# Kernel optimization log

Measured on AMD Instinct MI355X. Metric: run time of the kernel, lower is better.

## Reference

```python
import jax, jax.numpy as jnp
import numpy as np

N_NODES = 100000
N_EDGES = 1200000


def setup_inputs() -> dict:
    key = jax.random.key(0)
    k1, k2, k3, k4 = jax.random.split(key, 4)
    x = jax.random.normal(k1, (N_NODES, 64), dtype=jnp.float32)
    edge_index = jax.random.randint(k2, (2, N_EDGES), 0, N_NODES, dtype=jnp.int64)
    W1 = jax.random.normal(k3, (64, 64), dtype=jnp.float32) * (1.0 / np.sqrt(64))
    b1 = jnp.zeros((64,), dtype=jnp.float32)
    W2 = jax.random.normal(k4, (64, 32), dtype=jnp.float32) * (1.0 / np.sqrt(64))
    b2 = jnp.zeros((32,), dtype=jnp.float32)
    return {"x": x, "edge_index": edge_index, "W1": W1, "b1": b1, "W2": W2, "b2": b2}


def _gcn_layer(x, src, dst, norm, W, b, n_nodes):
    # x: [N, Fin]; src/dst: [E'] (with self-loops); norm: [E']
    h = x @ W                      # [N, Fout] -- linear transform first (PyG GCNConv)
    msg = h[src] * norm[:, None]   # gather + edge-wise scale, [E', Fout]
    out = jax.ops.segment_sum(msg, dst, num_segments=n_nodes)  # scatter-add
    return out + b


def _gcn_norm(edge_index, n_nodes):
    # add self-loops, then symmetric normalization D^{-1/2} A_hat D^{-1/2}
    loop = jnp.arange(n_nodes, dtype=edge_index.dtype)
    src = jnp.concatenate([edge_index[0], loop])
    dst = jnp.concatenate([edge_index[1], loop])
    ones = jnp.ones(src.shape[0], dtype=jnp.float32)
    deg = jax.ops.segment_sum(ones, dst, num_segments=n_nodes)  # in-degree incl. self-loop
    dinv = jnp.where(deg > 0, jax.lax.rsqrt(deg), 0.0)
    norm = dinv[src] * dinv[dst]
    return src, dst, norm


def reference(x, edge_index, W1, b1, W2, b2):
    n_nodes = x.shape[0]
    src, dst, norm = _gcn_norm(edge_index, n_nodes)
    h = _gcn_layer(x, src, dst, norm, W1, b1, n_nodes)   # op1: GCNConv(in, hidden)
    out = _gcn_layer(h, src, dst, norm, W2, b2, n_nodes) # op2: GCNConv(hidden, out)
    return out
```

## Files before the change

### kernel.cpp

```cpp
#include <hip/hip_runtime.h>


#define TPB 256
#define NPB 512
#define BCAP 8192
#define TILE_E 4096
#define W_ELL 20
#define EXT_W 24
#define OVCAP 512

typedef __attribute__((ext_vector_type(8))) short bf16x8;
typedef __attribute__((ext_vector_type(4))) float f32x4;

__device__ __forceinline__ float bf2f(unsigned short u) {
    unsigned int v = ((unsigned int)u) << 16;
    return __builtin_bit_cast(float, v);
}
__device__ __forceinline__ unsigned short f2bf(float f) {
    unsigned int u = __builtin_bit_cast(unsigned int, f);
    u += 0x7FFFu + ((u >> 16) & 1u);
    return (unsigned short)(u >> 16);
}
__device__ __forceinline__ int edge_val(const void* ei, int is64, long long idx) {
    if (is64) return (int)((const long long*)ei)[idx];
    return ((const int*)ei)[idx];
}

__global__ void k_detect(const unsigned int* __restrict__ w, int nelems, int* flag,
                         int* __restrict__ bucket_wp, int* __restrict__ ext_cnt,
                         unsigned short* __restrict__ T0b, unsigned short* __restrict__ T1b,
                         float* __restrict__ dinv, int n_nodes,
                         const float* __restrict__ W1, const float* __restrict__ W2,
                         const float* __restrict__ b1,
                         unsigned short* __restrict__ W12Tb, float* __restrict__ c1) {
    int t = threadIdx.x;
    if (blockIdx.x == 1) {
        __shared__ float W1s[64][64];
        __shared__ float W2s[64][32];
        for (int i = t; i < 4096; i += TPB) W1s[i >> 6][i & 63] = W1[i];
        for (int i = t; i < 2048; i += TPB) W2s[i >> 5][i & 31] = W2[i];
        __syncthreads();
        for (int i = t; i < 2048; i += TPB) {
            int f = i >> 6, k = i & 63;
            float acc = 0.f;
#pragma unroll
            for (int j = 0; j < 64; ++j) acc += W1s[k][j] * W2s[j][f];
            W12Tb[i] = f2bf(acc);
        }
        if (t < 32) {
            float acc = 0.f;
#pragma unroll
            for (int j = 0; j < 64; ++j) acc += b1[j] * W2s[j][t];
            c1[t] = acc;
        }
        return;
    }
    __shared__ unsigned int red[TPB];
    bucket_wp[t] = 0;
    if (t == 0) {
        *ext_cnt = 0;
        dinv[n_nodes] = 0.f;
    }
    if (t < 32) {
        T0b[(size_t)n_nodes * 32 + t] = 0;
        T1b[(size_t)n_nodes * 32 + t] = 0;
    }
    unsigned int acc = 0;
    int limit = nelems < 16384 ? nelems : 16384;
    for (int i = 1 + 2 * t; i < limit; i += 2 * TPB) acc |= w[i];
    red[t] = acc;
    __syncthreads();
    for (int s = TPB / 2; s > 0; s >>= 1) {
        if (t < s) red[t] |= red[t + s];
        __syncthreads();
    }
    if (t == 0) *flag = (red[0] == 0u) ? 1 : 0;
}

__launch_bounds__(512)
__global__ void k_binA(const void* __restrict__ ei, const int* __restrict__ flag, int E,
                       int nb, unsigned int* __restrict__ gstage, int* __restrict__ bucket_wp) {
    __shared__ int lcnt[256];
    __shared__ int lboff[256];
    __shared__ int lrank[256];
    __shared__ int gbase[256];
    __shared__ int sh[256];
    __shared__ unsigned int spair[TILE_E];
    __shared__ unsigned char sbuck[TILE_E];
    int is64 = *flag;
    int t = threadIdx.x;
    int base_e = blockIdx.x * TILE_E;
    int ne = E - base_e;
    if (ne > TILE_E) ne = TILE_E;

    if (t < 256) {
        lcnt[t] = 0;
        lrank[t] = 0;
    }
    __syncthreads();

    int myb[8];
    unsigned int mypair[8];
#pragma unroll
    for (int k = 0; k < 8; ++k) {
        int idx = t + k * 512;
        myb[k] = -1;
        if (idx < ne) {
            long long e = base_e + idx;
            int s = edge_val(ei, is64, e);
            int d = edge_val(ei, is64, (long long)E + e);
            int b = d >> 9;
            myb[k] = b;
            mypair[k] = (unsigned int)s | ((unsigned int)(d & (NPB - 1)) << 20);
            atomicAdd(&lcnt[b], 1);
        }
    }
    __syncthreads();

    int v0 = (t < 256) ? lcnt[t] : 0;
    if (t < 256) sh[t] = v0;
    __syncthreads();
    for (int st = 1; st < 256; st <<= 1) {
        int u = (t >= st && t < 256) ? sh[t - st] : 0;
        __syncthreads();
        if (t < 256) sh[t] += u;
        __syncthreads();
    }
    if (t < 256) {
        lboff[t] = sh[t] - v0;
        if (t < nb && v0 > 0) gbase[t] = atomicAdd(&bucket_wp[t], v0);
    }
    __syncthreads();

#pragma unroll
    for (int k = 0; k < 8; ++k) {
        int b = myb[k];
        if (b >= 0) {
            int r = atomicAdd(&lrank[b], 1);
            int slot = lboff[b] + r;
            spair[slot] = mypair[k];
            sbuck[slot] = (unsigned char)b;
        }
    }
    __syncthreads();

    for (int j = t; j < ne; j += 512) {
        int b = sbuck[j];
        int pos = gbase[b] + (j - lboff[b]);
        if (pos < BCAP) gstage[(size_t)b * BCAP + pos] = spair[j];
    }
}

__launch_bounds__(512)
__global__ void k_ellB(const unsigned int* __restrict__ gstage, const int* __restrict__ bucket_wp,
                       const float* __restrict__ x, const unsigned short* __restrict__ W12Tb,
                       int* __restrict__ ell, int* __restrict__ cnt, int* __restrict__ ext,
                       int* __restrict__ ext_cnt, float* __restrict__ dinv,
                       unsigned short* __restrict__ T0b, int n_nodes) {
    __shared__ int lrank[NPB];
    __shared__ int slab[NPB * W_ELL];
    __shared__ int exts[NPB];
    __shared__ float sdinv[NPB];
    __shared__ unsigned int ovfl[OVCAP];
    __shared__ int novf;
    int b = blockIdx.x, t = threadIdx.x;
    int zr = n_nodes;
    lrank[t] = 0;
    if (t == 0) novf = 0;
    int4 z4 = make_int4(zr, zr, zr, zr);
    for (int j = t; j < NPB * W_ELL / 4; j += 512) ((int4*)slab)[j] = z4;
    __syncthreads();
    int cb = bucket_wp[b];
    if (cb > BCAP) cb = BCAP;
    const unsigned int* gp = gstage + (size_t)b * BCAP;
    for (int j = t; j < cb; j += 512) {
        unsigned int w = gp[j];
        int dl = (int)(w >> 20);
        int r = atomicAdd(&lrank[dl], 1);
        if (r < W_ELL) {
            slab[dl * W_ELL + r] = (int)(w & 0xFFFFFu);
        } else {
            int o = atomicAdd(&novf, 1);
            if (o < OVCAP) ovfl[o] = w;
        }
    }
    __syncthreads();
    int node = b * NPB + t;
    int deg = lrank[t];
    int extrow = -1;
    if (node < n_nodes && deg > W_ELL) extrow = atomicAdd(ext_cnt, 1);
    exts[t] = extrow;
    float di = (node < n_nodes) ? rsqrtf((float)(deg + 1)) : 0.f;
    sdinv[t] = di;
    if (node < n_nodes) {
        cnt[node] = deg | ((extrow + 1) << 16);
        dinv[node] = di;
    }
    if (extrow >= 0) {
        int4* xp = (int4*)(ext + (size_t)extrow * EXT_W);
#pragma unroll
        for (int j = 0; j < EXT_W / 4; ++j) xp[j] = z4;
    }
    __syncthreads();
    lrank[t] = 0;
    __syncthreads();
    int nov = novf < OVCAP ? novf : OVCAP;
    for (int j = t; j < nov; j += 512) {
        unsigned int w = ovfl[j];
        int dl = (int)(w >> 20);
        int r2 = atomicAdd(&lrank[dl], 1);
        if (r2 < EXT_W) ext[(size_t)exts[dl] * EXT_W + r2] = (int)(w & 0xFFFFFu);
    }
    {
        int4* dst = (int4*)(ell + (size_t)b * (NPB * W_ELL));
        for (int j = t; j < NPB * W_ELL / 4; j += 512) dst[j] = ((int4*)slab)[j];
    }

    int w = t >> 6, lane = t & 63;
    int r = lane & 15, kb = lane >> 4;
#pragma unroll
    for (int ti = 0; ti < 4; ++ti) {
        int lbase = (w * 4 + ti) * 16;
        int nbase = b * NPB + lbase;
        if (nbase >= n_nodes) break;
        int ar = nbase + r;
        if (ar > n_nodes - 1) ar = n_nodes - 1;
        const float* xp = x + (size_t)ar * 64 + kb * 8;
        float4 v0 = ((const float4*)xp)[0];
        float4 v1 = ((const float4*)xp)[1];
        float4 v2 = ((const float4*)(xp + 32))[0];
        float4 v3 = ((const float4*)(xp + 32))[1];
        union { bf16x8 v; unsigned short e[8]; } a0, a1;
        a0.e[0] = f2bf(v0.x); a0.e[1] = f2bf(v0.y); a0.e[2] = f2bf(v0.z); a0.e[3] = f2bf(v0.w);
        a0.e[4] = f2bf(v1.x); a0.e[5] = f2bf(v1.y); a0.e[6] = f2bf(v1.z); a0.e[7] = f2bf(v1.w);
        a1.e[0] = f2bf(v2.x); a1.e[1] = f2bf(v2.y); a1.e[2] = f2bf(v2.z); a1.e[3] = f2bf(v2.w);
        a1.e[4] = f2bf(v3.x); a1.e[5] = f2bf(v3.y); a1.e[6] = f2bf(v3.z); a1.e[7] = f2bf(v3.w);
        int rl = lbase + 4 * kb;
        float d0 = sdinv[rl], d1 = sdinv[rl + 1], d2 = sdinv[rl + 2], d3 = sdinv[rl + 3];
        int rnode = b * NPB + rl;
#pragma unroll
        for (int ft = 0; ft < 2; ++ft) {
            const unsigned short* bp = W12Tb + (size_t)(ft * 16 + r) * 64 + kb * 8;
            bf16x8 b0 = *(const bf16x8*)bp;
            bf16x8 b1v = *(const bf16x8*)(bp + 32);
            f32x4 acc = {0.f, 0.f, 0.f, 0.f};
            acc = __builtin_amdgcn_mfma_f32_16x16x32_bf16(a0.v, b0, acc, 0, 0, 0);
            acc = __builtin_amdgcn_mfma_f32_16x16x32_bf16(a1.v, b1v, acc, 0, 0, 0);
            if (rnode + 0 < n_nodes) T0b[(size_t)(rnode + 0) * 32 + ft * 16 + r] = f2bf(acc[0] * d0);
            if (rnode + 1 < n_nodes) T0b[(size_t)(rnode + 1) * 32 + ft * 16 + r] = f2bf(acc[1] * d1);
            if (rnode + 2 < n_nodes) T0b[(size_t)(rnode + 2) * 32 + ft * 16 + r] = f2bf(acc[2] * d2);
            if (rnode + 3 < n_nodes) T0b[(size_t)(rnode + 3) * 32 + ft * 16 + r] = f2bf(acc[3] * d3);
        }
    }
}

#define GATH32(TBL, S)                                                         \
    {                                                                          \
        ushort4 u = ((const ushort4*)(TBL + (size_t)(S) * 32))[fl];            \
        a0 += bf2f(u.x); a1 += bf2f(u.y); a2 += bf2f(u.z); a3 += bf2f(u.w);    \
    }

__launch_bounds__(TPB)
__global__ void k_agg1(const int* __restrict__ ell, const int* __restrict__ ext,
                       const unsigned short* __restrict__ T0b, const float* __restrict__ dinv,
                       const int* __restrict__ cnt, unsigned short* __restrict__ T1b,
                       float* __restrict__ sraw, int n_nodes) {
    int t = threadIdx.x;
    int lane = t & 63;
    int g = lane >> 3, fl = lane & 7;
    int node = blockIdx.x * 32 + (t >> 6) * 8 + g;
    if (node >= n_nodes) return;
    int cw = cnt[node];
    int cv = cw & 0xFFFF;
    int er = (cw >> 16) - 1;
    const int* epi = ell + (size_t)node * W_ELL;
    const int4* ep = (const int4*)epi;
    int4 i0 = ep[0], i1 = ep[1], i2 = ep[2], i3 = ep[3];
    float sv = dinv[epi[fl]] + dinv[epi[8 + fl]];
    if (fl < 4) sv += dinv[epi[16 + fl]];
    ushort4 su = ((const ushort4*)(T0b + (size_t)node * 32))[fl];
    float a0 = bf2f(su.x), a1 = bf2f(su.y), a2 = bf2f(su.z), a3 = bf2f(su.w);
    GATH32(T0b, i0.x) GATH32(T0b, i0.y) GATH32(T0b, i0.z) GATH32(T0b, i0.w)
    GATH32(T0b, i1.x) GATH32(T0b, i1.y) GATH32(T0b, i1.z) GATH32(T0b, i1.w)
    GATH32(T0b, i2.x) GATH32(T0b, i2.y) GATH32(T0b, i2.z) GATH32(T0b, i2.w)
    GATH32(T0b, i3.x) GATH32(T0b, i3.y) GATH32(T0b, i3.z) GATH32(T0b, i3.w)
    if (__any(cv > 16)) {
        int4 i4 = ep[4];
        GATH32(T0b, i4.x) GATH32(T0b, i4.y) GATH32(T0b, i4.z) GATH32(T0b, i4.w)
    }
    if (er >= 0) {
        const int* xpi = ext + (size_t)er * EXT_W;
        const int4* xp = (const int4*)xpi;
        sv += dinv[xpi[fl]] + dinv[xpi[8 + fl]] + dinv[xpi[16 + fl]];
        int4 e0 = xp[0], e1 = xp[1], e2 = xp[2];
        int4 e3 = xp[3], e4 = xp[4], e5 = xp[5];
        GATH32(T0b, e0.x) GATH32(T0b, e0.y) GATH32(T0b, e0.z) GATH32(T0b, e0.w)
        GATH32(T0b, e1.x) GATH32(T0b, e1.y) GATH32(T0b, e1.z) GATH32(T0b, e1.w)
        GATH32(T0b, e2.x) GATH32(T0b, e2.y) GATH32(T0b, e2.z) GATH32(T0b, e2.w)
        GATH32(T0b, e3.x) GATH32(T0b, e3.y) GATH32(T0b, e3.z) GATH32(T0b, e3.w)
        GATH32(T0b, e4.x) GATH32(T0b, e4.y) GATH32(T0b, e4.z) GATH32(T0b, e4.w)
        GATH32(T0b, e5.x) GATH32(T0b, e5.y) GATH32(T0b, e5.z) GATH32(T0b, e5.w)
    }
    sv += __shfl_xor(sv, 1);
    sv += __shfl_xor(sv, 2);
    sv += __shfl_xor(sv, 4);
    float di = dinv[node];
    float d2 = di * di;
    ushort4 o;
    o.x = f2bf(d2 * a0);
    o.y = f2bf(d2 * a1);
    o.z = f2bf(d2 * a2);
    o.w = f2bf(d2 * a3);
    ((ushort4*)(T1b + (size_t)node * 32))[fl] = o;
    if (fl == 0) sraw[node] = sv + di;
}

__launch_bounds__(TPB)
__global__ void k_agg2(const int* __restrict__ ell, const int* __restrict__ ext,
                       const unsigned short* __restrict__ T1b, const float* __restrict__ dinv,
                       const int* __restrict__ cnt, const float* __restrict__ sraw,
                       const float* __restrict__ c1, const float* __restrict__ b2,
                       float* __restrict__ out, int n_nodes) {
    int t = threadIdx.x;
    int lane = t & 63;
    int g = lane >> 3, fl = lane & 7;
    int node = blockIdx.x * 32 + (t >> 6) * 8 + g;
    if (node >= n_nodes) return;
    int cw = cnt[node];
    int cv = cw & 0xFFFF;
    int er = (cw >> 16) - 1;
    const int4* ep = (const int4*)(ell + (size_t)node * W_ELL);
    int4 i0 = ep[0], i1 = ep[1], i2 = ep[2], i3 = ep[3];
    ushort4 su = ((const ushort4*)(T1b + (size_t)node * 32))[fl];
    float a0 = bf2f(su.x), a1 = bf2f(su.y), a2 = bf2f(su.z), a3 = bf2f(su.w);
    GATH32(T1b, i0.x) GATH32(T1b, i0.y) GATH32(T1b, i0.z) GATH32(T1b, i0.w)
    GATH32(T1b, i1.x) GATH32(T1b, i1.y) GATH32(T1b, i1.z) GATH32(T1b, i1.w)
    GATH32(T1b, i2.x) GATH32(T1b, i2.y) GATH32(T1b, i2.z) GATH32(T1b, i2.w)
    GATH32(T1b, i3.x) GATH32(T1b, i3.y) GATH32(T1b, i3.z) GATH32(T1b, i3.w)
    if (__any(cv > 16)) {
        int4 i4 = ep[4];
        GATH32(T1b, i4.x) GATH32(T1b, i4.y) GATH32(T1b, i4.z) GATH32(T1b, i4.w)
    }
    if (er >= 0) {
        const int4* xp = (const int4*)(ext + (size_t)er * EXT_W);
        int4 e0 = xp[0], e1 = xp[1], e2 = xp[2];
        int4 e3 = xp[3], e4 = xp[4], e5 = xp[5];
        GATH32(T1b, e0.x) GATH32(T1b, e0.y) GATH32(T1b, e0.z) GATH32(T1b, e0.w)
        GATH32(T1b, e1.x) GATH32(T1b, e1.y) GATH32(T1b, e1.z) GATH32(T1b, e1.w)
        GATH32(T1b, e2.x) GATH32(T1b, e2.y) GATH32(T1b, e2.z) GATH32(T1b, e2.w)
        GATH32(T1b, e3.x) GATH32(T1b, e3.y) GATH32(T1b, e3.z) GATH32(T1b, e3.w)
        GATH32(T1b, e4.x) GATH32(T1b, e4.y) GATH32(T1b, e4.z) GATH32(T1b, e4.w)
        GATH32(T1b, e5.x) GATH32(T1b, e5.y) GATH32(T1b, e5.z) GATH32(T1b, e5.w)
    }
    float di = dinv[node];
    float sv = sraw[node];
    float4 cc = ((const float4*)c1)[fl];
    float4 bb = ((const float4*)b2)[fl];
    float4 o;
    o.x = di * (a0 + sv * cc.x) + bb.x;
    o.y = di * (a1 + sv * cc.y) + bb.y;
    o.z = di * (a2 + sv * cc.z) + bb.z;
    o.w = di * (a3 + sv * cc.w) + bb.w;
    ((float4*)(out + (size_t)node * 32))[fl] = o;
}

extern "C" void kernel_launch(void* const* d_in, const int* in_sizes, int n_in,
                              void* d_out, int out_size, void* d_ws, size_t ws_size,
                              hipStream_t stream) {
    const float* x  = (const float*)d_in[0];
    const void*  ei = d_in[1];
    const float* W1 = (const float*)d_in[2];
    const float* b1 = (const float*)d_in[3];
    const float* W2 = (const float*)d_in[4];
    const float* b2 = (const float*)d_in[5];
    float* out = (float*)d_out;

    const int n_nodes = in_sizes[0] / 64;
    const int E = in_sizes[1] / 2;
    const int nb = (n_nodes + NPB - 1) / NPB;

    char* p = (char*)d_ws;
    auto carve = [&](size_t bytes) {
        char* r = p;
        p += (bytes + 255) / 256 * 256;
        return r;
    };
    int* flag      = (int*)carve(sizeof(int));
    int* bucket_wp = (int*)carve(256 * sizeof(int));
    int* ext_cnt   = (int*)carve(sizeof(int));
    int* cnt       = (int*)carve((size_t)n_nodes * sizeof(int));
    float* dinv    = (float*)carve(((size_t)n_nodes + 1) * sizeof(float));
    float* sraw    = (float*)carve((size_t)n_nodes * sizeof(float));
    unsigned int* gstage = (unsigned int*)carve((size_t)nb * BCAP * sizeof(unsigned int));
    int* ell       = (int*)carve((size_t)nb * NPB * W_ELL * sizeof(int));
    int* ext       = (int*)carve((size_t)16384 * EXT_W * sizeof(int));
    unsigned short* T0b = (unsigned short*)carve(((size_t)n_nodes + 1) * 32 * sizeof(unsigned short));
    unsigned short* T1b = (unsigned short*)carve(((size_t)n_nodes + 1) * 32 * sizeof(unsigned short));
    unsigned short* W12Tb = (unsigned short*)carve(32 * 64 * sizeof(unsigned short));
    float* c1      = (float*)carve(32 * sizeof(float));

    k_detect<<<2, TPB, 0, stream>>>((const unsigned int*)ei, in_sizes[1], flag, bucket_wp,
                                    ext_cnt, T0b, T1b, dinv, n_nodes, W1, W2, b1, W12Tb, c1);
    k_binA<<<(E + TILE_E - 1) / TILE_E, 512, 0, stream>>>(ei, flag, E, nb, gstage, bucket_wp);
    k_ellB<<<nb, 512, 0, stream>>>(gstage, bucket_wp, x, W12Tb, ell, cnt, ext, ext_cnt,
                                   dinv, T0b, n_nodes);
    k_agg1<<<(n_nodes + 31) / 32, TPB, 0, stream>>>(ell, ext, T0b, dinv, cnt, T1b, sraw,
                                                    n_nodes);
    k_agg2<<<(n_nodes + 31) / 32, TPB, 0, stream>>>(ell, ext, T1b, dinv, cnt, sraw, c1,
                                                    b2, out, n_nodes);
}
```

Baseline: 95.53 us.

## Drop detect kernel, fold weight prep into ELL build, widen gather lanes

Removes the separate detect kernel. Index width is now detected per block inside the binning kernel, the counters are zeroed with a memset, and every ELL block recomputes the W1·W2 product into shared memory instead of reading it from a global buffer. The aggregation kernels now have each lane gather 8 bf16 features (16-byte loads) with 4 lanes per node, so each block covers 64 nodes instead of 32. This saves a launch and halves the number of gather instructions per edge, at the cost of redundant small matmuls in every ELL block and more registers per lane.

Result: slower. 110.9 us (+16.0%).

```diff
diff --git a/kernel.cpp b/kernel.cpp
--- a/kernel.cpp
+++ b/kernel.cpp
@@ -10,6 +10,7 @@
 #define OVCAP 512
 
 typedef __attribute__((ext_vector_type(8))) short bf16x8;
+typedef __attribute__((ext_vector_type(8))) unsigned short u16x8;
 typedef __attribute__((ext_vector_type(4))) float f32x4;
 
 __device__ __forceinline__ float bf2f(unsigned short u) {
@@ -26,60 +27,9 @@
     return ((const int*)ei)[idx];
 }
 
-__global__ void k_detect(const unsigned int* __restrict__ w, int nelems, int* flag,
-                         int* __restrict__ bucket_wp, int* __restrict__ ext_cnt,
-                         unsigned short* __restrict__ T0b, unsigned short* __restrict__ T1b,
-                         float* __restrict__ dinv, int n_nodes,
-                         const float* __restrict__ W1, const float* __restrict__ W2,
-                         const float* __restrict__ b1,
-                         unsigned short* __restrict__ W12Tb, float* __restrict__ c1) {
-    int t = threadIdx.x;
-    if (blockIdx.x == 1) {
-        __shared__ float W1s[64][64];
-        __shared__ float W2s[64][32];
-        for (int i = t; i < 4096; i += TPB) W1s[i >> 6][i & 63] = W1[i];
-        for (int i = t; i < 2048; i += TPB) W2s[i >> 5][i & 31] = W2[i];
-        __syncthreads();
-        for (int i = t; i < 2048; i += TPB) {
-            int f = i >> 6, k = i & 63;
-            float acc = 0.f;
-#pragma unroll
-            for (int j = 0; j < 64; ++j) acc += W1s[k][j] * W2s[j][f];
-            W12Tb[i] = f2bf(acc);
-        }
-        if (t < 32) {
-            float acc = 0.f;
-#pragma unroll
-            for (int j = 0; j < 64; ++j) acc += b1[j] * W2s[j][t];
-            c1[t] = acc;
-        }
-        return;
-    }
-    __shared__ unsigned int red[TPB];
-    bucket_wp[t] = 0;
-    if (t == 0) {
-        *ext_cnt = 0;
-        dinv[n_nodes] = 0.f;
-    }
-    if (t < 32) {
-        T0b[(size_t)n_nodes * 32 + t] = 0;
-        T1b[(size_t)n_nodes * 32 + t] = 0;
-    }
-    unsigned int acc = 0;
-    int limit = nelems < 16384 ? nelems : 16384;
-    for (int i = 1 + 2 * t; i < limit; i += 2 * TPB) acc |= w[i];
-    red[t] = acc;
-    __syncthreads();
-    for (int s = TPB / 2; s > 0; s >>= 1) {
-        if (t < s) red[t] |= red[t + s];
-        __syncthreads();
-    }
-    if (t == 0) *flag = (red[0] == 0u) ? 1 : 0;
-}
-
 __launch_bounds__(512)
-__global__ void k_binA(const void* __restrict__ ei, const int* __restrict__ flag, int E,
-                       int nb, unsigned int* __restrict__ gstage, int* __restrict__ bucket_wp) {
+__global__ void k_binA(const void* __restrict__ ei, int E, int nb,
+                       unsigned int* __restrict__ gstage, int* __restrict__ bucket_wp) {
     __shared__ int lcnt[256];
     __shared__ int lboff[256];
     __shared__ int lrank[256];
@@ -87,17 +37,25 @@
     __shared__ int sh[256];
     __shared__ unsigned int spair[TILE_E];
     __shared__ unsigned char sbuck[TILE_E];
-    int is64 = *flag;
+    __shared__ int s_is32;
     int t = threadIdx.x;
     int base_e = blockIdx.x * TILE_E;
     int ne = E - base_e;
     if (ne > TILE_E) ne = TILE_E;
 
+    unsigned int det = 0;
+    int lim = ne < 2048 ? ne : 2048;
+    if (t == 0) s_is32 = 0;
+    for (int j = t; j < lim; j += 512)
+        det |= ((const unsigned int*)ei)[((size_t)(base_e + j)) * 2 + 1];
     if (t < 256) {
         lcnt[t] = 0;
         lrank[t] = 0;
     }
     __syncthreads();
+    if (det != 0) s_is32 = 1;
+    __syncthreads();
+    int is64 = s_is32 ? 0 : 1;
 
     int myb[8];
     unsigned int mypair[8];
@@ -153,15 +111,18 @@
 
 __launch_bounds__(512)
 __global__ void k_ellB(const unsigned int* __restrict__ gstage, const int* __restrict__ bucket_wp,
-                       const float* __restrict__ x, const unsigned short* __restrict__ W12Tb,
+                       const float* __restrict__ x, const float* __restrict__ W1,
+                       const float* __restrict__ W2, const float* __restrict__ b1,
                        int* __restrict__ ell, int* __restrict__ cnt, int* __restrict__ ext,
                        int* __restrict__ ext_cnt, float* __restrict__ dinv,
-                       unsigned short* __restrict__ T0b, int n_nodes) {
+                       unsigned short* __restrict__ T0b, unsigned short* __restrict__ T1b,
+                       float* __restrict__ c1, int n_nodes) {
     __shared__ int lrank[NPB];
     __shared__ int slab[NPB * W_ELL];
     __shared__ int exts[NPB];
     __shared__ float sdinv[NPB];
     __shared__ unsigned int ovfl[OVCAP];
+    __shared__ unsigned short W12s[32 * 64];
     __shared__ int novf;
     int b = blockIdx.x, t = threadIdx.x;
     int zr = n_nodes;
@@ -215,6 +176,32 @@
         int4* dst = (int4*)(ell + (size_t)b * (NPB * W_ELL));
         for (int j = t; j < NPB * W_ELL / 4; j += 512) dst[j] = ((int4*)slab)[j];
     }
+    __syncthreads();
+
+    float* W1s = (float*)slab;
+    float* W2s = (float*)slab + 4096;
+    for (int i = t; i < 4096; i += 512) W1s[i] = W1[i];
+    for (int i = t; i < 2048; i += 512) W2s[i] = W2[i];
+    __syncthreads();
+    for (int i = t; i < 2048; i += 512) {
+        int f = i >> 6, k = i & 63;
+        float acc = 0.f;
+#pragma unroll
+        for (int j = 0; j < 64; ++j) acc += W1s[k * 64 + j] * W2s[j * 32 + f];
+        W12s[i] = f2bf(acc);
+    }
+    if (b == 0) {
+        if (t < 32) {
+            float acc = 0.f;
+#pragma unroll
+            for (int j = 0; j < 64; ++j) acc += b1[j] * W2s[j * 32 + t];
+            c1[t] = acc;
+            T0b[(size_t)n_nodes * 32 + t] = 0;
+            T1b[(size_t)n_nodes * 32 + t] = 0;
+        }
+        if (t == 0) dinv[n_nodes] = 0.f;
+    }
+    __syncthreads();
 
     int w = t >> 6, lane = t & 63;
     int r = lane & 15, kb = lane >> 4;
@@ -240,7 +227,7 @@
         int rnode = b * NPB + rl;
 #pragma unroll
         for (int ft = 0; ft < 2; ++ft) {
-            const unsigned short* bp = W12Tb + (size_t)(ft * 16 + r) * 64 + kb * 8;
+            const unsigned short* bp = W12s + (ft * 16 + r) * 64 + kb * 8;
             bf16x8 b0 = *(const bf16x8*)bp;
             bf16x8 b1v = *(const bf16x8*)(bp + 32);
             f32x4 acc = {0.f, 0.f, 0.f, 0.f};
@@ -254,10 +241,11 @@
     }
 }
 
-#define GATH32(TBL, S)                                                         \
+#define GATH8(TBL, S)                                                          \
     {                                                                          \
-        ushort4 u = ((const ushort4*)(TBL + (size_t)(S) * 32))[fl];            \
-        a0 += bf2f(u.x); a1 += bf2f(u.y); a2 += bf2f(u.z); a3 += bf2f(u.w);    \
+        u16x8 u = *(const u16x8*)((TBL) + (size_t)(S) * 32 + fl * 8);          \
+        a0 += bf2f(u[0]); a1 += bf2f(u[1]); a2 += bf2f(u[2]); a3 += bf2f(u[3]);\
+        a4 += bf2f(u[4]); a5 += bf2f(u[5]); a6 += bf2f(u[6]); a7 += bf2f(u[7]);\
     }
 
 __launch_bounds__(TPB)
@@ -267,8 +255,8 @@
                        float* __restrict__ sraw, int n_nodes) {
     int t = threadIdx.x;
     int lane = t & 63;
-    int g = lane >> 3, fl = lane & 7;
-    int node = blockIdx.x * 32 + (t >> 6) * 8 + g;
+    int g = lane >> 2, fl = lane & 3;
+    int node = blockIdx.x * 64 + (t >> 6) * 16 + g;
     if (node >= n_nodes) return;
     int cw = cnt[node];
     int cv = cw & 0xFFFF;
@@ -276,42 +264,41 @@
     const int* epi = ell + (size_t)node * W_ELL;
     const int4* ep = (const int4*)epi;
     int4 i0 = ep[0], i1 = ep[1], i2 = ep[2], i3 = ep[3];
-    float sv = dinv[epi[fl]] + dinv[epi[8 + fl]];
-    if (fl < 4) sv += dinv[epi[16 + fl]];
-    ushort4 su = ((const ushort4*)(T0b + (size_t)node * 32))[fl];
-    float a0 = bf2f(su.x), a1 = bf2f(su.y), a2 = bf2f(su.z), a3 = bf2f(su.w);
-    GATH32(T0b, i0.x) GATH32(T0b, i0.y) GATH32(T0b, i0.z) GATH32(T0b, i0.w)
-    GATH32(T0b, i1.x) GATH32(T0b, i1.y) GATH32(T0b, i1.z) GATH32(T0b, i1.w)
-    GATH32(T0b, i2.x) GATH32(T0b, i2.y) GATH32(T0b, i2.z) GATH32(T0b, i2.w)
-    GATH32(T0b, i3.x) GATH32(T0b, i3.y) GATH32(T0b, i3.z) GATH32(T0b, i3.w)
+    float sv = dinv[epi[fl]] + dinv[epi[4 + fl]] + dinv[epi[8 + fl]] + dinv[epi[12 + fl]]
+             + dinv[epi[16 + fl]];
+    u16x8 su = *(const u16x8*)(T0b + (size_t)node * 32 + fl * 8);
+    float a0 = bf2f(su[0]), a1 = bf2f(su[1]), a2 = bf2f(su[2]), a3 = bf2f(su[3]);
+    float a4 = bf2f(su[4]), a5 = bf2f(su[5]), a6 = bf2f(su[6]), a7 = bf2f(su[7]);
+    GATH8(T0b, i0.x) GATH8(T0b, i0.y) GATH8(T0b, i0.z) GATH8(T0b, i0.w)
+    GATH8(T0b, i1.x) GATH8(T0b, i1.y) GATH8(T0b, i1.z) GATH8(T0b, i1.w)
+    GATH8(T0b, i2.x) GATH8(T0b, i2.y) GATH8(T0b, i2.z) GATH8(T0b, i2.w)
+    GATH8(T0b, i3.x) GATH8(T0b, i3.y) GATH8(T0b, i3.z) GATH8(T0b, i3.w)
     if (__any(cv > 16)) {
         int4 i4 = ep[4];
-        GATH32(T0b, i4.x) GATH32(T0b, i4.y) GATH32(T0b, i4.z) GATH32(T0b, i4.w)
+        GATH8(T0b, i4.x) GATH8(T0b, i4.y) GATH8(T0b, i4.z) GATH8(T0b, i4.w)
     }
     if (er >= 0) {
         const int* xpi = ext + (size_t)er * EXT_W;
         const int4* xp = (const int4*)xpi;
-        sv += dinv[xpi[fl]] + dinv[xpi[8 + fl]] + dinv[xpi[16 + fl]];
+        sv += dinv[xpi[fl]] + dinv[xpi[4 + fl]] + dinv[xpi[8 + fl]] + dinv[xpi[12 + fl]]
+            + dinv[xpi[16 + fl]] + dinv[xpi[20 + fl]];
         int4 e0 = xp[0], e1 = xp[1], e2 = xp[2];
         int4 e3 = xp[3], e4 = xp[4], e5 = xp[5];
-        GATH32(T0b, e0.x) GATH32(T0b, e0.y) GATH32(T0b, e0.z) GATH32(T0b, e0.w)
-        GATH32(T0b, e1.x) GATH32(T0b, e1.y) GATH32(T0b, e1.z) GATH32(T0b, e1.w)
-        GATH32(T0b, e2.x) GATH32(T0b, e2.y) GATH32(T0b, e2.z) GATH32(T0b, e2.w)
-        GATH32(T0b, e3.x) GATH32(T0b, e3.y) GATH32(T0b, e3.z) GATH32(T0b, e3.w)
-        GATH32(T0b, e4.x) GATH32(T0b, e4.y) GATH32(T0b, e4.z) GATH32(T0b, e4.w)
-        GATH32(T0b, e5.x) GATH32(T0b, e5.y) GATH32(T0b, e5.z) GATH32(T0b, e5.w)
+        GATH8(T0b, e0.x) GATH8(T0b, e0.y) GATH8(T0b, e0.z) GATH8(T0b, e0.w)
+        GATH8(T0b, e1.x) GATH8(T0b, e1.y) GATH8(T0b, e1.z) GATH8(T0b, e1.w)
+        GATH8(T0b, e2.x) GATH8(T0b, e2.y) GATH8(T0b, e2.z) GATH8(T0b, e2.w)
+        GATH8(T0b, e3.x) GATH8(T0b, e3.y) GATH8(T0b, e3.z) GATH8(T0b, e3.w)
+        GATH8(T0b, e4.x) GATH8(T0b, e4.y) GATH8(T0b, e4.z) GATH8(T0b, e4.w)
+        GATH8(T0b, e5.x) GATH8(T0b, e5.y) GATH8(T0b, e5.z) GATH8(T0b, e5.w)
     }
     sv += __shfl_xor(sv, 1);
     sv += __shfl_xor(sv, 2);
-    sv += __shfl_xor(sv, 4);
     float di = dinv[node];
     float d2 = di * di;
-    ushort4 o;
-    o.x = f2bf(d2 * a0);
-    o.y = f2bf(d2 * a1);
-    o.z = f2bf(d2 * a2);
-    o.w = f2bf(d2 * a3);
-    ((ushort4*)(T1b + (size_t)node * 32))[fl] = o;
+    u16x8 o;
+    o[0] = f2bf(d2 * a0); o[1] = f2bf(d2 * a1); o[2] = f2bf(d2 * a2); o[3] = f2bf(d2 * a3);
+    o[4] = f2bf(d2 * a4); o[5] = f2bf(d2 * a5); o[6] = f2bf(d2 * a6); o[7] = f2bf(d2 * a7);
+    *(u16x8*)(T1b + (size_t)node * 32 + fl * 8) = o;
     if (fl == 0) sraw[node] = sv + di;
 }
 
@@ -323,45 +310,53 @@
                        float* __restrict__ out, int n_nodes) {
     int t = threadIdx.x;
     int lane = t & 63;
-    int g = lane >> 3, fl = lane & 7;
-    int node = blockIdx.x * 32 + (t >> 6) * 8 + g;
+    int g = lane >> 2, fl = lane & 3;
+    int node = blockIdx.x * 64 + (t >> 6) * 16 + g;
     if (node >= n_nodes) return;
     int cw = cnt[node];
     int cv = cw & 0xFFFF;
     int er = (cw >> 16) - 1;
     const int4* ep = (const int4*)(ell + (size_t)node * W_ELL);
     int4 i0 = ep[0], i1 = ep[1], i2 = ep[2], i3 = ep[3];
-    ushort4 su = ((const ushort4*)(T1b + (size_t)node * 32))[fl];
-    float a0 = bf2f(su.x), a1 = bf2f(su.y), a2 = bf2f(su.z), a3 = bf2f(su.w);
-    GATH32(T1b, i0.x) GATH32(T1b, i0.y) GATH32(T1b, i0.z) GATH32(T1b, i0.w)
-    GATH32(T1b, i1.x) GATH32(T1b, i1.y) GATH32(T1b, i1.z) GATH32(T1b, i1.w)
-    GATH32(T1b, i2.x) GATH32(T1b, i2.y) GATH32(T1b, i2.z) GATH32(T1b, i2.w)
-    GATH32(T1b, i3.x) GATH32(T1b, i3.y) GATH32(T1b, i3.z) GATH32(T1b, i3.w)
+    u16x8 su = *(const u16x8*)(T1b + (size_t)node * 32 + fl * 8);
+    float a0 = bf2f(su[0]), a1 = bf2f(su[1]), a2 = bf2f(su[2]), a3 = bf2f(su[3]);
+    float a4 = bf2f(su[4]), a5 = bf2f(su[5]), a6 = bf2f(su[6]), a7 = bf2f(su[7]);
+    GATH8(T1b, i0.x) GATH8(T1b, i0.y) GATH8(T1b, i0.z) GATH8(T1b, i0.w)
+    GATH8(T1b, i1.x) GATH8(T1b, i1.y) GATH8(T1b, i1.z) GATH8(T1b, i1.w)
+    GATH8(T1b, i2.x) GATH8(T1b, i2.y) GATH8(T1b, i2.z) GATH8(T1b, i2.w)
+    GATH8(T1b, i3.x) GATH8(T1b, i3.y) GATH8(T1b, i3.z) GATH8(T1b, i3.w)
     if (__any(cv > 16)) {
         int4 i4 = ep[4];
-        GATH32(T1b, i4.x) GATH32(T1b, i4.y) GATH32(T1b, i4.z) GATH32(T1b, i4.w)
+        GATH8(T1b, i4.x) GATH8(T1b, i4.y) GATH8(T1b, i4.z) GATH8(T1b, i4.w)
     }
     if (er >= 0) {
         const int4* xp = (const int4*)(ext + (size_t)er * EXT_W);
         int4 e0 = xp[0], e1 = xp[1], e2 = xp[2];
         int4 e3 = xp[3], e4 = xp[4], e5 = xp[5];
-        GATH32(T1b, e0.x) GATH32(T1b, e0.y) GATH32(T1b, e0.z) GATH32(T1b, e0.w)
-        GATH32(T1b, e1.x) GATH32(T1b, e1.y) GATH32(T1b, e1.z) GATH32(T1b, e1.w)
-        GATH32(T1b, e2.x) GATH32(T1b, e2.y) GATH32(T1b, e2.z) GATH32(T1b, e2.w)
-        GATH32(T1b, e3.x) GATH32(T1b, e3.y) GATH32(T1b, e3.z) GATH32(T1b, e3.w)
-        GATH32(T1b, e4.x) GATH32(T1b, e4.y) GATH32(T1b, e4.z) GATH32(T1b, e4.w)
-        GATH32(T1b, e5.x) GATH32(T1b, e5.y) GATH32(T1b, e5.z) GATH32(T1b, e5.w)
+        GATH8(T1b, e0.x) GATH8(T1b, e0.y) GATH8(T1b, e0.z) GATH8(T1b, e0.w)
+        GATH8(T1b, e1.x) GATH8(T1b, e1.y) GATH8(T1b, e1.z) GATH8(T1b, e1.w)
+        GATH8(T1b, e2.x) GATH8(T1b, e2.y) GATH8(T1b, e2.z) GATH8(T1b, e2.w)
+        GATH8(T1b, e3.x) GATH8(T1b, e3.y) GATH8(T1b, e3.z) GATH8(T1b, e3.w)
+        GATH8(T1b, e4.x) GATH8(T1b, e4.y) GATH8(T1b, e4.z) GATH8(T1b, e4.w)
+        GATH8(T1b, e5.x) GATH8(T1b, e5.y) GATH8(T1b, e5.z) GATH8(T1b, e5.w)
     }
     float di = dinv[node];
     float sv = sraw[node];
-    float4 cc = ((const float4*)c1)[fl];
-    float4 bb = ((const float4*)b2)[fl];
-    float4 o;
-    o.x = di * (a0 + sv * cc.x) + bb.x;
-    o.y = di * (a1 + sv * cc.y) + bb.y;
-    o.z = di * (a2 + sv * cc.z) + bb.z;
-    o.w = di * (a3 + sv * cc.w) + bb.w;
-    ((float4*)(out + (size_t)node * 32))[fl] = o;
+    float4 cc0 = ((const float4*)c1)[fl * 2];
+    float4 cc1 = ((const float4*)c1)[fl * 2 + 1];
+    float4 bb0 = ((const float4*)b2)[fl * 2];
+    float4 bb1 = ((const float4*)b2)[fl * 2 + 1];
+    float4 o0, o1;
+    o0.x = di * (a0 + sv * cc0.x) + bb0.x;
+    o0.y = di * (a1 + sv * cc0.y) + bb0.y;
+    o0.z = di * (a2 + sv * cc0.z) + bb0.z;
+    o0.w = di * (a3 + sv * cc0.w) + bb0.w;
+    o1.x = di * (a4 + sv * cc1.x) + bb1.x;
+    o1.y = di * (a5 + sv * cc1.y) + bb1.y;
+    o1.z = di * (a6 + sv * cc1.z) + bb1.z;
+    o1.w = di * (a7 + sv * cc1.w) + bb1.w;
+    ((float4*)(out + (size_t)node * 32))[fl * 2] = o0;
+    ((float4*)(out + (size_t)node * 32))[fl * 2 + 1] = o1;
 }
 
 extern "C" void kernel_launch(void* const* d_in, const int* in_sizes, int n_in,
@@ -385,9 +380,8 @@
         p += (bytes + 255) / 256 * 256;
         return r;
     };
-    int* flag      = (int*)carve(sizeof(int));
-    int* bucket_wp = (int*)carve(256 * sizeof(int));
-    int* ext_cnt   = (int*)carve(sizeof(int));
+    int* bucket_wp = (int*)carve(257 * sizeof(int));
+    int* ext_cnt   = bucket_wp + 256;
     int* cnt       = (int*)carve((size_t)n_nodes * sizeof(int));
     float* dinv    = (float*)carve(((size_t)n_nodes + 1) * sizeof(float));
     float* sraw    = (float*)carve((size_t)n_nodes * sizeof(float));
@@ -396,16 +390,14 @@
     int* ext       = (int*)carve((size_t)16384 * EXT_W * sizeof(int));
     unsigned short* T0b = (unsigned short*)carve(((size_t)n_nodes + 1) * 32 * sizeof(unsigned short));
     unsigned short* T1b = (unsigned short*)carve(((size_t)n_nodes + 1) * 32 * sizeof(unsigned short));
-    unsigned short* W12Tb = (unsigned short*)carve(32 * 64 * sizeof(unsigned short));
     float* c1      = (float*)carve(32 * sizeof(float));
 
-    k_detect<<<2, TPB, 0, stream>>>((const unsigned int*)ei, in_sizes[1], flag, bucket_wp,
-                                    ext_cnt, T0b, T1b, dinv, n_nodes, W1, W2, b1, W12Tb, c1);
-    k_binA<<<(E + TILE_E - 1) / TILE_E, 512, 0, stream>>>(ei, flag, E, nb, gstage, bucket_wp);
-    k_ellB<<<nb, 512, 0, stream>>>(gstage, bucket_wp, x, W12Tb, ell, cnt, ext, ext_cnt,
-                                   dinv, T0b, n_nodes);
-    k_agg1<<<(n_nodes + 31) / 32, TPB, 0, stream>>>(ell, ext, T0b, dinv, cnt, T1b, sraw,
+    hipMemsetAsync(bucket_wp, 0, 257 * sizeof(int), stream);
+    k_binA<<<(E + TILE_E - 1) / TILE_E, 512, 0, stream>>>(ei, E, nb, gstage, bucket_wp);
+    k_ellB<<<nb, 512, 0, stream>>>(gstage, bucket_wp, x, W1, W2, b1, ell, cnt, ext, ext_cnt,
+                                   dinv, T0b, T1b, c1, n_nodes);
+    k_agg1<<<(n_nodes + 63) / 64, TPB, 0, stream>>>(ell, ext, T0b, dinv, cnt, T1b, sraw,
                                                     n_nodes);
-    k_agg2<<<(n_nodes + 31) / 32, TPB, 0, stream>>>(ell, ext, T1b, dinv, cnt, sraw, c1,
+    k_agg2<<<(n_nodes + 63) / 64, TPB, 0, stream>>>(ell, ext, T1b, dinv, cnt, sraw, c1,
                                                     b2, out, n_nodes);
 }
```
